# Optimization experiments

Measured on AMD Instinct MI355X. Metric: run time of the kernel, lower is better.

Reference implementation:

```python
import jax, jax.numpy as jnp
import numpy as np

B, N, DIM, H = 512, 98, 512, 16
HD = DIM // H
WS = (2, 7, 7)  # window size; N == 2*7*7


def _relative_position_index(ws):
    d, h, w = ws
    coords = np.stack(np.meshgrid(np.arange(d), np.arange(h), np.arange(w), indexing='ij'))
    cf = coords.reshape(3, -1)  # [3, N]
    rel = cf[:, :, None] - cf[:, None, :]  # [3, N, N]
    rel = rel.transpose(1, 2, 0).astype(np.int64)
    rel[:, :, 0] += d - 1
    rel[:, :, 1] += h - 1
    rel[:, :, 2] += w - 1
    rel[:, :, 0] *= (2 * h - 1) * (2 * w - 1)
    rel[:, :, 1] *= 2 * w - 1
    return rel.sum(-1)  # [N, N] in [0, (2d-1)(2h-1)(2w-1))


def setup_inputs() -> dict:
    key = jax.random.key(0)
    ks = jax.random.split(key, 6)
    table_size = (2 * WS[0] - 1) * (2 * WS[1] - 1) * (2 * WS[2] - 1)  # 507
    return {
        'x': jax.random.normal(ks[0], (B, N, DIM), jnp.float32),
        'qkv_w': jax.random.normal(ks[1], (DIM, 3 * DIM), jnp.float32) * 0.02,
        'qkv_b': jnp.zeros((3 * DIM,), jnp.float32),
        'proj_w': jax.random.normal(ks[2], (DIM, DIM), jnp.float32) * 0.02,
        'proj_b': jnp.zeros((DIM,), jnp.float32),
        'bias_table': jax.random.normal(ks[3], (table_size, H), jnp.float32) * 0.02,
        'rel_index': jnp.asarray(_relative_position_index(WS)),
    }


def reference(x, qkv_w, qkv_b, proj_w, proj_b, bias_table, rel_index):
    b, n, c = x.shape
    scale = HD ** -0.5
    qkv = (x @ qkv_w + qkv_b).reshape(b, n, 3, H, HD)
    qkv = jnp.transpose(qkv, (2, 0, 3, 1, 4))  # [3, B, H, N, HD]
    q, k, v = qkv[0] * scale, qkv[1], qkv[2]
    attn = jnp.einsum('bhnd,bhmd->bhnm', q, k)  # [B, H, N, N]
    # gather relative position bias: [N,N] indices into [table, H] -> [H, N, N]
    bias = jnp.transpose(bias_table[rel_index], (2, 0, 1))
    attn = jax.nn.softmax(attn + bias[None], axis=-1)
    out = jnp.einsum('bhnm,bhmd->bhnd', attn, v)  # [B, H, N, HD]
    out = jnp.transpose(out, (0, 2, 1, 3)).reshape(b, n, c)
    return out @ proj_w + proj_b
```

## Files before the change

kernel.cpp:

```cpp
#include <hip/hip_runtime.h>

typedef unsigned short u16;
typedef __bf16 bf16x8 __attribute__((ext_vector_type(8)));
typedef float f32x4 __attribute__((ext_vector_type(4)));

typedef __attribute__((address_space(1))) const void* as1_cvp;
typedef __attribute__((address_space(3))) void* as3_vp;

__device__ __forceinline__ float b2f(u16 u) {
  union { unsigned int i; float f; } x; x.i = ((unsigned int)u) << 16; return x.f;
}
__device__ __forceinline__ u16 f2b(float f) {
  union { float f; unsigned int i; } x; x.f = f;
  unsigned int u = x.i;
  u += 0x7fffu + ((u >> 16) & 1u);
  return (u16)(u >> 16);
}

__global__ void k_detect(const u16* __restrict__ x, int* __restrict__ flag) {
  int t = threadIdx.x;
  int sane = 0;
#pragma unroll
  for (int i = 0; i < 8; ++i) {
    u16 u = x[t * 8 + i];
    int e = (u >> 7) & 0xFF;
    sane += (u == 0 || (e >= 100 && e <= 150)) ? 1 : 0;
  }
#pragma unroll
  for (int off = 32; off >= 1; off >>= 1) sane += __shfl_xor(sane, off);
  if (t == 0) *flag = (sane < 480) ? 1 : 0;
}

__global__ void k_convert(const void* __restrict__ xin, u16* __restrict__ xb,
                          const int* __restrict__ flagp) {
  if (!*flagp) return;
  long i = ((long)blockIdx.x * 256 + threadIdx.x) * 4;
  float4 v = *(const float4*)((const float*)xin + i);
  u16* o = xb + i;
  o[0] = f2b(v.x); o[1] = f2b(v.y); o[2] = f2b(v.z); o[3] = f2b(v.w);
}

__global__ void k_transpose(const void* __restrict__ W, u16* __restrict__ WT,
                            const int* __restrict__ flagp, int K, int N) {
  __shared__ u16 tile[32][33];
  int f = *flagp;
  int n0 = blockIdx.x * 32, k0 = blockIdx.y * 32;
  int tx = threadIdx.x, ty = threadIdx.y;
#pragma unroll
  for (int i = 0; i < 32; i += 8) {
    long idx = (long)(k0 + ty + i) * N + n0 + tx;
    tile[ty + i][tx] = f ? f2b(((const float*)W)[idx]) : ((const u16*)W)[idx];
  }
  __syncthreads();
#pragma unroll
  for (int i = 0; i < 32; i += 8)
    WT[(long)(n0 + ty + i) * K + k0 + tx] = tile[tx][ty + i];
}

__global__ void k_biasfrag(const int* __restrict__ rel, const void* __restrict__ table,
                           u16* __restrict__ biasFrag, const int* __restrict__ flagp) {
  int t = blockIdx.x * 256 + threadIdx.x;
  int f = *flagp;
  int ln = t & 63, r2 = t >> 6;
  int tj = r2 & 7, r3 = r2 >> 3;
  int ti = r3 % 7, h = r3 / 7;
  int col = ln & 15, qrow = ln >> 4;
  int j = tj * 16 + col;
  u16 v[4];
#pragma unroll
  for (int r = 0; r < 4; ++r) {
    int i = ti * 16 + qrow * 4 + r; if (i > 97) i = 97;
    float val;
    if (j < 98) {
      int rr = rel[i * 98 + j];
      val = f ? ((const float*)table)[rr * 16 + h] : b2f(((const u16*)table)[rr * 16 + h]);
    } else {
      val = -1e30f;
    }
    v[r] = f2b(val);
  }
  ushort4 out; out.x = v[0]; out.y = v[1]; out.z = v[2]; out.w = v[3];
  *(ushort4*)(biasFrag + (long)t * 4) = out;
}

__global__ __launch_bounds__(256) void k_gemm_bt(
    const u16* __restrict__ A_raw, const u16* __restrict__ A_conv,
    const u16* __restrict__ BT, const void* __restrict__ bias, void* __restrict__ C,
    const int* __restrict__ flagp, int N, int K, int out_follows_flag) {
  __shared__ __align__(16) u16 As[128 * 32];
  __shared__ __align__(16) u16 Bs[128 * 32];
  const int f = *flagp;
  const u16* A = f ? A_conv : A_raw;
  const int t = threadIdx.x, w = t >> 6, ln = t & 63;
  const long bm = (long)blockIdx.x * 128, bn = (long)blockIdx.y * 128;
  const int lrow = ln >> 2, lseg = ln & 3;
  const u16* ag0 = A + (bm + w * 32 + lrow) * (long)K + lseg * 8;
  const u16* ag1 = ag0 + 16L * K;
  const u16* bg0 = BT + (bn + w * 32 + lrow) * (long)K + lseg * 8;
  const u16* bg1 = bg0 + 16L * K;
  u16* As0 = &As[w * 1024]; u16* As1 = &As[w * 1024 + 512];
  u16* Bs0 = &Bs[w * 1024]; u16* Bs1 = &Bs[w * 1024 + 512];
  const int wm = w & 1, wn = w >> 1;
  const int col = ln & 15, qrow = ln >> 4;
  f32x4 acc[4][4] = {};
  for (int k0 = 0; k0 < K; k0 += 32) {
    __syncthreads();
    __builtin_amdgcn_global_load_lds((as1_cvp)(const void*)(ag0 + k0), (as3_vp)As0, 16, 0, 0);
    __builtin_amdgcn_global_load_lds((as1_cvp)(const void*)(ag1 + k0), (as3_vp)As1, 16, 0, 0);
    __builtin_amdgcn_global_load_lds((as1_cvp)(const void*)(bg0 + k0), (as3_vp)Bs0, 16, 0, 0);
    __builtin_amdgcn_global_load_lds((as1_cvp)(const void*)(bg1 + k0), (as3_vp)Bs1, 16, 0, 0);
    __syncthreads();
    bf16x8 af[4], bfr[4];
#pragma unroll
    for (int mi = 0; mi < 4; ++mi)
      af[mi] = *(const bf16x8*)&As[(wm * 64 + mi * 16 + col) * 32 + qrow * 8];
#pragma unroll
    for (int ni = 0; ni < 4; ++ni)
      bfr[ni] = *(const bf16x8*)&Bs[(wn * 64 + ni * 16 + col) * 32 + qrow * 8];
#pragma unroll
    for (int mi = 0; mi < 4; ++mi)
#pragma unroll
      for (int ni = 0; ni < 4; ++ni)
        acc[mi][ni] = __builtin_amdgcn_mfma_f32_16x16x32_bf16(af[mi], bfr[ni], acc[mi][ni], 0, 0, 0);
  }
  const int of = out_follows_flag ? f : 0;
  float bv[4];
#pragma unroll
  for (int ni = 0; ni < 4; ++ni) {
    long c = bn + wn * 64 + ni * 16 + col;
    bv[ni] = f ? ((const float*)bias)[c] : b2f(((const u16*)bias)[c]);
  }
#pragma unroll
  for (int mi = 0; mi < 4; ++mi)
#pragma unroll
    for (int ni = 0; ni < 4; ++ni)
#pragma unroll
      for (int r = 0; r < 4; ++r) {
        long row = bm + wm * 64 + mi * 16 + qrow * 4 + r;
        long c = bn + wn * 64 + ni * 16 + col;
        float v = acc[mi][ni][r] + bv[ni];
        if (of) ((float*)C)[row * N + c] = v;
        else    ((u16*)C)[row * N + c] = f2b(v);
      }
}

__global__ __launch_bounds__(256) void k_attn(
    const u16* __restrict__ qkv, const u16* __restrict__ biasFrag,
    u16* __restrict__ attnout) {
  __shared__ __align__(16) u16 Qs[112 * 32];
  __shared__ __align__(16) u16 Ks[128 * 32];
  __shared__ __align__(16) u16 Vt[32 * 136];
  __shared__ __align__(16) u16 Ps[4][16 * 136];
  const int b = blockIdx.x, h = blockIdx.y;
  const int t = threadIdx.x, w = t >> 6, ln = t & 63;
  const u16* qbase = qkv + (long)b * 98 * 1536 + h * 32;
  {
    const int gr = ln >> 2, gc = (ln & 3) * 8;
    for (int n = w; n < 7; n += 4) {
      int g = n * 16 + gr; if (g > 97) g = 97;
      __builtin_amdgcn_global_load_lds((as1_cvp)(const void*)(qbase + (long)g * 1536 + gc),
                                       (as3_vp)(Qs + n * 512), 16, 0, 0);
    }
    for (int n = w; n < 8; n += 4) {
      int g = n * 16 + gr; if (g > 97) g = 97;
      __builtin_amdgcn_global_load_lds((as1_cvp)(const void*)(qbase + 512 + (long)g * 1536 + gc),
                                       (as3_vp)(Ks + n * 512), 16, 0, 0);
    }
  }
  for (int z = t; z < 32 * 19; z += 256) {
    int d = z / 19, q = z % 19;
    *(unsigned int*)&Vt[d * 136 + 98 + q * 2] = 0u;
  }
  for (int idx = t; idx < 784; idx += 256) {
    int i = idx >> 3, c4 = (idx & 7) * 4;
    ushort4 v4 = *(const ushort4*)(qbase + 1024 + (long)i * 1536 + c4);
    Vt[(c4 + 0) * 136 + i] = v4.x;
    Vt[(c4 + 1) * 136 + i] = v4.y;
    Vt[(c4 + 2) * 136 + i] = v4.z;
    Vt[(c4 + 3) * 136 + i] = v4.w;
  }
  __syncthreads();
  const int col = ln & 15, qrow = ln >> 4;
  const float scale = 0.17677669529663687f;
  u16* Psw = &Ps[w][0];
  f32x4 o[2][2] = {{{0.f,0.f,0.f,0.f},{0.f,0.f,0.f,0.f}},{{0.f,0.f,0.f,0.f},{0.f,0.f,0.f,0.f}}};
  for (int tt = 0; tt < 2; ++tt) {
    const int ti = w + tt * 4;
    if (ti >= 7) break;
    const u16* bp = biasFrag + ((long)((h * 7 + ti) * 8) * 64 + ln) * 4;
    ushort4 bfv[8];
#pragma unroll
    for (int tj = 0; tj < 8; ++tj) bfv[tj] = *(const ushort4*)(bp + tj * 256);
    bf16x8 aq = *(const bf16x8*)&Qs[(ti * 16 + col) * 32 + qrow * 8];
    f32x4 s[8];
#pragma unroll
    for (int tj = 0; tj < 8; ++tj) {
      bf16x8 bk = *(const bf16x8*)&Ks[(tj * 16 + col) * 32 + qrow * 8];
      f32x4 z = {0.f, 0.f, 0.f, 0.f};
      s[tj] = __builtin_amdgcn_mfma_f32_16x16x32_bf16(aq, bk, z, 0, 0, 0);
    }
#pragma unroll
    for (int r = 0; r < 4; ++r) {
      float vals[8]; float m = -1e30f;
#pragma unroll
      for (int tj = 0; tj < 8; ++tj) {
        u16 bb = (r == 0) ? bfv[tj].x : (r == 1) ? bfv[tj].y : (r == 2) ? bfv[tj].z : bfv[tj].w;
        float v = fmaf(s[tj][r], scale, b2f(bb));
        vals[tj] = v; m = fmaxf(m, v);
      }
#pragma unroll
      for (int off = 1; off < 16; off <<= 1) m = fmaxf(m, __shfl_xor(m, off));
      float sum = 0.f;
#pragma unroll
      for (int tj = 0; tj < 8; ++tj) { vals[tj] = __expf(vals[tj] - m); sum += vals[tj]; }
#pragma unroll
      for (int off = 1; off < 16; off <<= 1) sum += __shfl_xor(sum, off);
      float inv = 1.f / sum;
      const int rt = qrow * 4 + r;
#pragma unroll
      for (int tj = 0; tj < 8; ++tj)
        Psw[rt * 136 + tj * 16 + col] = f2b(vals[tj] * inv);
    }
#pragma unroll
    for (int ks = 0; ks < 4; ++ks) {
      bf16x8 ap  = *(const bf16x8*)&Psw[col * 136 + ks * 32 + qrow * 8];
      bf16x8 bv0 = *(const bf16x8*)&Vt[col * 136 + ks * 32 + qrow * 8];
      bf16x8 bv1 = *(const bf16x8*)&Vt[(16 + col) * 136 + ks * 32 + qrow * 8];
      o[tt][0] = __builtin_amdgcn_mfma_f32_16x16x32_bf16(ap, bv0, o[tt][0], 0, 0, 0);
      o[tt][1] = __builtin_amdgcn_mfma_f32_16x16x32_bf16(ap, bv1, o[tt][1], 0, 0, 0);
    }
  }
  __syncthreads();
  u16* Os = Qs;
#pragma unroll
  for (int tt = 0; tt < 2; ++tt) {
    const int ti = w + tt * 4;
    if (ti >= 7) continue;
#pragma unroll
    for (int r = 0; r < 4; ++r) {
      const int i = ti * 16 + qrow * 4 + r;
      if (i < 98) {
        Os[i * 32 + col]      = f2b(o[tt][0][r]);
        Os[i * 32 + 16 + col] = f2b(o[tt][1][r]);
      }
    }
  }
  __syncthreads();
  u16* obase = attnout + (long)b * 98 * 512 + h * 32;
  for (int idx = t; idx < 784; idx += 256) {
    int i = idx >> 3, c4 = (idx & 7) * 4;
    *(ushort4*)(obase + (long)i * 512 + c4) = *(const ushort4*)&Os[i * 32 + c4];
  }
}

extern "C" void kernel_launch(void* const* d_in, const int* in_sizes, int n_in,
                              void* d_out, int out_size, void* d_ws, size_t ws_size,
                              hipStream_t stream) {
  (void)in_sizes; (void)n_in; (void)out_size; (void)ws_size;
  char* p = (char*)d_ws;
  u16* qkvbuf   = (u16*)p;  p += 50176L * 1536 * 2;
  u16* attnbuf  = (u16*)p;  u16* xb = attnbuf; p += 50176L * 512 * 2;
  u16* wqkvT    = (u16*)p;  p += 1536L * 512 * 2;
  u16* wprojT   = (u16*)p;  p += 512L * 512 * 2;
  u16* biasFrag = (u16*)p;  p += 57344L * 4 * 2;
  int* flagp    = (int*)p;

  k_detect<<<1, 64, 0, stream>>>((const u16*)d_in[0], flagp);
  k_convert<<<25088, 256, 0, stream>>>(d_in[0], xb, flagp);
  k_transpose<<<dim3(48, 16), dim3(32, 8), 0, stream>>>(d_in[1], wqkvT, flagp, 512, 1536);
  k_transpose<<<dim3(16, 16), dim3(32, 8), 0, stream>>>(d_in[3], wprojT, flagp, 512, 512);
  k_biasfrag<<<224, 256, 0, stream>>>((const int*)d_in[6], d_in[5], biasFrag, flagp);
  k_gemm_bt<<<dim3(392, 12), 256, 0, stream>>>((const u16*)d_in[0], xb, wqkvT, d_in[2],
                                               qkvbuf, flagp, 1536, 512, 0);
  k_attn<<<dim3(512, 16), 256, 0, stream>>>(qkvbuf, biasFrag, attnbuf);
  k_gemm_bt<<<dim3(392, 4), 256, 0, stream>>>(attnbuf, attnbuf, wprojT, d_in[4],
                                              d_out, flagp, 512, 512, 1);
}
```

Before: 476.0 us.

## Replace GEMM with 256x256 tiled, double-buffered, swizzled-LDS pipelined kernel

Rewrites the GEMM used for the QKV and output projections. It now uses 256x256 block tiles with 8 waves and a K-step of 64, double-buffers LDS and issues async global-to-LDS prefetches interleaved with MFMA quadrants. It also uses an XOR swizzle on LDS chunks to avoid bank conflicts, raises MFMA issue priority with s_setprio, and remaps workgroups across XCDs. The goal is to cut the per-k-step barrier stalls and reload overhead of the old 128x128 single-buffer kernel, at the cost of heavier LDS use (128KB per block), more register pressure and fragile hand-placed waitcnt sequencing.

```diff
diff --git a/kernel.cpp b/kernel.cpp
--- a/kernel.cpp
+++ b/kernel.cpp
@@ -83,60 +83,111 @@
   *(ushort4*)(biasFrag + (long)t * 4) = out;
 }
 
-__global__ __launch_bounds__(256) void k_gemm_bt(
+#define MFMA_Q(M0, N0)                                                         \
+  __builtin_amdgcn_s_setprio(1);                                               \
+  _Pragma("unroll") for (int mi = 0; mi < 4; ++mi)                             \
+  _Pragma("unroll") for (int ni = 0; ni < 2; ++ni)                             \
+  _Pragma("unroll") for (int kk = 0; kk < 2; ++kk)                             \
+      acc[(M0) + mi][(N0) + ni] = __builtin_amdgcn_mfma_f32_16x16x32_bf16(     \
+          afr[mi][kk], bfr[(N0) + ni][kk], acc[(M0) + mi][(N0) + ni], 0, 0, 0);\
+  __builtin_amdgcn_s_setprio(0);
+
+#define STAGE(arr, bufi, half, src, kt) do {                                   \
+    u16* _d = &arr[(bufi) * 16384 + (half) * 8192 + w * 512];                  \
+    const u16* _s = (src) + (long)(half) * 128 * K + (long)(kt) * 64;          \
+    __builtin_amdgcn_global_load_lds((as1_cvp)(const void*)_s, (as3_vp)_d, 16, 0, 0); \
+    __builtin_amdgcn_global_load_lds((as1_cvp)(const void*)(_s + 64L * K),     \
+                                     (as3_vp)(_d + 4096), 16, 0, 0);           \
+  } while (0)
+
+__global__ __launch_bounds__(512, 2) void k_gemm256(
     const u16* __restrict__ A_raw, const u16* __restrict__ A_conv,
     const u16* __restrict__ BT, const void* __restrict__ bias, void* __restrict__ C,
-    const int* __restrict__ flagp, int N, int K, int out_follows_flag) {
-  __shared__ __align__(16) u16 As[128 * 32];
-  __shared__ __align__(16) u16 Bs[128 * 32];
+    const int* __restrict__ flagp, int N, int K, int out_follows_flag, int NBY) {
+  __shared__ __align__(16) u16 As[32768];
+  __shared__ __align__(16) u16 Bs[32768];
   const int f = *flagp;
   const u16* A = f ? A_conv : A_raw;
   const int t = threadIdx.x, w = t >> 6, ln = t & 63;
-  const long bm = (long)blockIdx.x * 128, bn = (long)blockIdx.y * 128;
-  const int lrow = ln >> 2, lseg = ln & 3;
-  const u16* ag0 = A + (bm + w * 32 + lrow) * (long)K + lseg * 8;
-  const u16* ag1 = ag0 + 16L * K;
-  const u16* bg0 = BT + (bn + w * 32 + lrow) * (long)K + lseg * 8;
-  const u16* bg1 = bg0 + 16L * K;
-  u16* As0 = &As[w * 1024]; u16* As1 = &As[w * 1024 + 512];
-  u16* Bs0 = &Bs[w * 1024]; u16* Bs1 = &Bs[w * 1024 + 512];
-  const int wm = w & 1, wn = w >> 1;
-  const int col = ln & 15, qrow = ln >> 4;
-  f32x4 acc[4][4] = {};
-  for (int k0 = 0; k0 < K; k0 += 32) {
-    __syncthreads();
-    __builtin_amdgcn_global_load_lds((as1_cvp)(const void*)(ag0 + k0), (as3_vp)As0, 16, 0, 0);
-    __builtin_amdgcn_global_load_lds((as1_cvp)(const void*)(ag1 + k0), (as3_vp)As1, 16, 0, 0);
-    __builtin_amdgcn_global_load_lds((as1_cvp)(const void*)(bg0 + k0), (as3_vp)Bs0, 16, 0, 0);
-    __builtin_amdgcn_global_load_lds((as1_cvp)(const void*)(bg1 + k0), (as3_vp)Bs1, 16, 0, 0);
-    __syncthreads();
-    bf16x8 af[4], bfr[4];
-#pragma unroll
-    for (int mi = 0; mi < 4; ++mi)
-      af[mi] = *(const bf16x8*)&As[(wm * 64 + mi * 16 + col) * 32 + qrow * 8];
-#pragma unroll
-    for (int ni = 0; ni < 4; ++ni)
-      bfr[ni] = *(const bf16x8*)&Bs[(wn * 64 + ni * 16 + col) * 32 + qrow * 8];
-#pragma unroll
-    for (int mi = 0; mi < 4; ++mi)
-#pragma unroll
-      for (int ni = 0; ni < 4; ++ni)
-        acc[mi][ni] = __builtin_amdgcn_mfma_f32_16x16x32_bf16(af[mi], bfr[ni], acc[mi][ni], 0, 0, 0);
-  }
-  const int of = out_follows_flag ? f : 0;
+  const int nwg = gridDim.x, cpx = nwg >> 3;
+  const int wg = (blockIdx.x & 7) * cpx + (blockIdx.x >> 3);
+  const long bm = (long)(wg / NBY) * 256, bn = (long)(wg % NBY) * 256;
+  const int NK = K >> 6;
+  const int wm = w >> 2, wn = w & 3, bh = wn >> 1, bq = wn & 1;
+  const int col = ln & 15, qrow = ln >> 4, cx = ln & 7;
+  const int srow = w * 8 + (ln >> 3);
+  const int schunk = (ln & 7) ^ ((ln >> 3) & 7);
+  const u16* aS = A + (bm + srow) * (long)K + schunk * 8;
+  const u16* bS = BT + (bn + srow) * (long)K + schunk * 8;
+  const u16* aRd = &As[wm * 8192 + col * 64];
+  const u16* bRd = &Bs[bh * 8192 + bq * 4096 + col * 64];
+  const int ko0 = (qrow ^ cx) * 8;
+  const int ko1 = ((4 + qrow) ^ cx) * 8;
   float bv[4];
 #pragma unroll
   for (int ni = 0; ni < 4; ++ni) {
     long c = bn + wn * 64 + ni * 16 + col;
     bv[ni] = f ? ((const float*)bias)[c] : b2f(((const u16*)bias)[c]);
   }
-#pragma unroll
-  for (int mi = 0; mi < 4; ++mi)
+  asm volatile("" ::: "memory");
+  STAGE(Bs, 0, 0, bS, 0); STAGE(Bs, 0, 1, bS, 0);
+  STAGE(As, 0, 0, aS, 0); STAGE(As, 0, 1, aS, 0);
+  STAGE(Bs, 1, 0, bS, 1); STAGE(Bs, 1, 1, bS, 1);
+  STAGE(As, 1, 0, aS, 1);
+  asm volatile("s_waitcnt vmcnt(6)" ::: "memory");
+  __builtin_amdgcn_s_barrier();
+
+  f32x4 acc[8][4] = {};
+  bf16x8 afr[4][2], bfr[4][2];
+  for (int kt = 0; kt < NK; ++kt) {
+    const int buf = kt & 1;
+    const u16* aP = aRd + buf * 16384;
+    const u16* bP = bRd + buf * 16384;
+#pragma unroll
+    for (int i = 0; i < 4; ++i) {
+      afr[i][0] = *(const bf16x8*)(aP + i * 1024 + ko0);
+      afr[i][1] = *(const bf16x8*)(aP + i * 1024 + ko1);
+      bfr[i][0] = *(const bf16x8*)(bP + i * 1024 + ko0);
+      bfr[i][1] = *(const bf16x8*)(bP + i * 1024 + ko1);
+    }
+    if (kt + 1 < NK) STAGE(As, buf ^ 1, 1, aS, kt + 1);
+    __builtin_amdgcn_s_barrier();
+    MFMA_Q(0, 0)
+    asm volatile("s_waitcnt lgkmcnt(0)" ::: "memory");
+    __builtin_amdgcn_s_barrier();
+    if (kt + 2 < NK) STAGE(Bs, buf, 0, bS, kt + 2);
+    __builtin_amdgcn_s_barrier();
+    MFMA_Q(0, 2)
+    asm volatile("s_waitcnt lgkmcnt(0)" ::: "memory");
+    __builtin_amdgcn_s_barrier();
+#pragma unroll
+    for (int i = 0; i < 4; ++i) {
+      afr[i][0] = *(const bf16x8*)(aP + (i + 4) * 1024 + ko0);
+      afr[i][1] = *(const bf16x8*)(aP + (i + 4) * 1024 + ko1);
+    }
+    if (kt + 2 < NK) STAGE(Bs, buf, 1, bS, kt + 2);
+    __builtin_amdgcn_s_barrier();
+    MFMA_Q(4, 0)
+    asm volatile("s_waitcnt lgkmcnt(0)" ::: "memory");
+    __builtin_amdgcn_s_barrier();
+    if (kt + 2 < NK) {
+      STAGE(As, buf, 0, aS, kt + 2);
+      asm volatile("s_waitcnt vmcnt(6)" ::: "memory");
+    } else if (kt + 1 < NK) {
+      asm volatile("s_waitcnt vmcnt(0)" ::: "memory");
+    }
+    __builtin_amdgcn_s_barrier();
+    MFMA_Q(4, 2)
+    __builtin_amdgcn_s_barrier();
+  }
+  const int of = out_follows_flag ? f : 0;
+#pragma unroll
+  for (int mi = 0; mi < 8; ++mi)
 #pragma unroll
     for (int ni = 0; ni < 4; ++ni)
 #pragma unroll
       for (int r = 0; r < 4; ++r) {
-        long row = bm + wm * 64 + mi * 16 + qrow * 4 + r;
+        long row = bm + wm * 128 + mi * 16 + qrow * 4 + r;
         long c = bn + wn * 64 + ni * 16 + col;
         float v = acc[mi][ni][r] + bv[ni];
         if (of) ((float*)C)[row * N + c] = v;
@@ -270,9 +321,9 @@
   k_transpose<<<dim3(48, 16), dim3(32, 8), 0, stream>>>(d_in[1], wqkvT, flagp, 512, 1536);
   k_transpose<<<dim3(16, 16), dim3(32, 8), 0, stream>>>(d_in[3], wprojT, flagp, 512, 512);
   k_biasfrag<<<224, 256, 0, stream>>>((const int*)d_in[6], d_in[5], biasFrag, flagp);
-  k_gemm_bt<<<dim3(392, 12), 256, 0, stream>>>((const u16*)d_in[0], xb, wqkvT, d_in[2],
-                                               qkvbuf, flagp, 1536, 512, 0);
+  k_gemm256<<<dim3(196 * 6), 512, 0, stream>>>((const u16*)d_in[0], xb, wqkvT, d_in[2],
+                                               qkvbuf, flagp, 1536, 512, 0, 6);
   k_attn<<<dim3(512, 16), 256, 0, stream>>>(qkvbuf, biasFrag, attnbuf);
-  k_gemm_bt<<<dim3(392, 4), 256, 0, stream>>>(attnbuf, attnbuf, wprojT, d_in[4],
-                                              d_out, flagp, 512, 512, 1);
-}
+  k_gemm256<<<dim3(196 * 2), 512, 0, stream>>>(attnbuf, attnbuf, wprojT, d_in[4],
+                                               d_out, flagp, 512, 512, 1, 2);
+}
```

Result: faster. 444.9 us (-6.5%).

## Rewrite GEMM with double-buffered K=64 LDS tiles, XOR swizzle, and XCD remap

Applied to the files above, without the earlier changes.

Replaces the single-buffered K=32 GEMM with a double-buffered K=64 pipeline that issues global-to-LDS loads two tiles ahead and waits on vmcnt before each barrier. LDS rows are XOR-swizzled to avoid bank conflicts on fragment reads. A 1D grid is remapped so consecutive tiles land on the same XCD, and launch bounds request two blocks per CU. This aims to overlap memory latency with MFMA work and cut the number of barriers, at the cost of 64KB of LDS per block and hand-written waitcnt logic.

```diff
diff --git a/kernel.cpp b/kernel.cpp
--- a/kernel.cpp
+++ b/kernel.cpp
@@ -83,53 +83,88 @@
   *(ushort4*)(biasFrag + (long)t * 4) = out;
 }
 
-__global__ __launch_bounds__(256) void k_gemm_bt(
+#define STAGE4(arr, bufi, src, kt) do {                                        \
+    u16* _d = &arr[(bufi) * 8192 + w * 512];                                   \
+    const u16* _s = (src) + (long)(kt) * 64;                                   \
+    __builtin_amdgcn_global_load_lds((as1_cvp)(const void*)(_s),           (as3_vp)(_d),        16, 0, 0); \
+    __builtin_amdgcn_global_load_lds((as1_cvp)(const void*)(_s + 32L * K), (as3_vp)(_d + 2048), 16, 0, 0); \
+    __builtin_amdgcn_global_load_lds((as1_cvp)(const void*)(_s + 64L * K), (as3_vp)(_d + 4096), 16, 0, 0); \
+    __builtin_amdgcn_global_load_lds((as1_cvp)(const void*)(_s + 96L * K), (as3_vp)(_d + 6144), 16, 0, 0); \
+  } while (0)
+
+__global__ __launch_bounds__(256, 2) void k_gemm128(
     const u16* __restrict__ A_raw, const u16* __restrict__ A_conv,
     const u16* __restrict__ BT, const void* __restrict__ bias, void* __restrict__ C,
-    const int* __restrict__ flagp, int N, int K, int out_follows_flag) {
-  __shared__ __align__(16) u16 As[128 * 32];
-  __shared__ __align__(16) u16 Bs[128 * 32];
+    const int* __restrict__ flagp, int N, int K, int out_follows_flag, int NBY) {
+  __shared__ __align__(16) u16 As[16384];
+  __shared__ __align__(16) u16 Bs[16384];
   const int f = *flagp;
   const u16* A = f ? A_conv : A_raw;
   const int t = threadIdx.x, w = t >> 6, ln = t & 63;
-  const long bm = (long)blockIdx.x * 128, bn = (long)blockIdx.y * 128;
-  const int lrow = ln >> 2, lseg = ln & 3;
-  const u16* ag0 = A + (bm + w * 32 + lrow) * (long)K + lseg * 8;
-  const u16* ag1 = ag0 + 16L * K;
-  const u16* bg0 = BT + (bn + w * 32 + lrow) * (long)K + lseg * 8;
-  const u16* bg1 = bg0 + 16L * K;
-  u16* As0 = &As[w * 1024]; u16* As1 = &As[w * 1024 + 512];
-  u16* Bs0 = &Bs[w * 1024]; u16* Bs1 = &Bs[w * 1024 + 512];
-  const int wm = w & 1, wn = w >> 1;
-  const int col = ln & 15, qrow = ln >> 4;
-  f32x4 acc[4][4] = {};
-  for (int k0 = 0; k0 < K; k0 += 32) {
-    __syncthreads();
-    __builtin_amdgcn_global_load_lds((as1_cvp)(const void*)(ag0 + k0), (as3_vp)As0, 16, 0, 0);
-    __builtin_amdgcn_global_load_lds((as1_cvp)(const void*)(ag1 + k0), (as3_vp)As1, 16, 0, 0);
-    __builtin_amdgcn_global_load_lds((as1_cvp)(const void*)(bg0 + k0), (as3_vp)Bs0, 16, 0, 0);
-    __builtin_amdgcn_global_load_lds((as1_cvp)(const void*)(bg1 + k0), (as3_vp)Bs1, 16, 0, 0);
-    __syncthreads();
-    bf16x8 af[4], bfr[4];
-#pragma unroll
-    for (int mi = 0; mi < 4; ++mi)
-      af[mi] = *(const bf16x8*)&As[(wm * 64 + mi * 16 + col) * 32 + qrow * 8];
-#pragma unroll
-    for (int ni = 0; ni < 4; ++ni)
-      bfr[ni] = *(const bf16x8*)&Bs[(wn * 64 + ni * 16 + col) * 32 + qrow * 8];
-#pragma unroll
-    for (int mi = 0; mi < 4; ++mi)
-#pragma unroll
-      for (int ni = 0; ni < 4; ++ni)
-        acc[mi][ni] = __builtin_amdgcn_mfma_f32_16x16x32_bf16(af[mi], bfr[ni], acc[mi][ni], 0, 0, 0);
-  }
-  const int of = out_follows_flag ? f : 0;
+  const int nwg = gridDim.x, cpx = nwg >> 3;
+  const int wg = (blockIdx.x & 7) * cpx + (blockIdx.x >> 3);
+  const long bm = (long)(wg / NBY) * 128, bn = (long)(wg % NBY) * 128;
+  const int NK = K >> 6;
+  const int wm = w >> 1, wn = w & 1;
+  const int col = ln & 15, qrow = ln >> 4, c7 = ln & 7;
+  const int srow = w * 8 + (ln >> 3);
+  const int schunk = (ln & 7) ^ ((ln >> 3) & 7);
+  const u16* aS = A + (bm + srow) * (long)K + schunk * 8;
+  const u16* bS = BT + (bn + srow) * (long)K + schunk * 8;
+  const u16* aRd = &As[(wm * 64 + col) * 64];
+  const u16* bRd = &Bs[(wn * 64 + col) * 64];
+  const int kc7 = col & 7;
+  const int ko0 = (qrow ^ kc7) * 8;
+  const int ko1 = ((4 + qrow) ^ kc7) * 8;
+  (void)c7;
   float bv[4];
 #pragma unroll
   for (int ni = 0; ni < 4; ++ni) {
     long c = bn + wn * 64 + ni * 16 + col;
     bv[ni] = f ? ((const float*)bias)[c] : b2f(((const u16*)bias)[c]);
   }
+  asm volatile("" ::: "memory");
+  STAGE4(As, 0, aS, 0); STAGE4(Bs, 0, bS, 0);
+  STAGE4(As, 1, aS, 1); STAGE4(Bs, 1, bS, 1);
+  asm volatile("s_waitcnt vmcnt(8)" ::: "memory");
+  __builtin_amdgcn_s_barrier();
+
+  f32x4 acc[4][4] = {};
+  for (int kt = 0; kt < NK; ++kt) {
+    const int buf = kt & 1;
+    const u16* aP = aRd + buf * 8192;
+    const u16* bP = bRd + buf * 8192;
+    bf16x8 a0[4], b0[4], a1[4], b1[4];
+#pragma unroll
+    for (int i = 0; i < 4; ++i) {
+      a0[i] = *(const bf16x8*)(aP + i * 1024 + ko0);
+      b0[i] = *(const bf16x8*)(bP + i * 1024 + ko0);
+      a1[i] = *(const bf16x8*)(aP + i * 1024 + ko1);
+      b1[i] = *(const bf16x8*)(bP + i * 1024 + ko1);
+    }
+    __builtin_amdgcn_s_setprio(1);
+#pragma unroll
+    for (int mi = 0; mi < 4; ++mi)
+#pragma unroll
+      for (int ni = 0; ni < 4; ++ni)
+        acc[mi][ni] = __builtin_amdgcn_mfma_f32_16x16x32_bf16(a0[mi], b0[ni], acc[mi][ni], 0, 0, 0);
+#pragma unroll
+    for (int mi = 0; mi < 4; ++mi)
+#pragma unroll
+      for (int ni = 0; ni < 4; ++ni)
+        acc[mi][ni] = __builtin_amdgcn_mfma_f32_16x16x32_bf16(a1[mi], b1[ni], acc[mi][ni], 0, 0, 0);
+    __builtin_amdgcn_s_setprio(0);
+    asm volatile("s_waitcnt lgkmcnt(0)" ::: "memory");
+    __builtin_amdgcn_s_barrier();
+    if (kt + 2 < NK) {
+      STAGE4(As, buf, aS, kt + 2); STAGE4(Bs, buf, bS, kt + 2);
+      asm volatile("s_waitcnt vmcnt(8)" ::: "memory");
+    } else if (kt + 1 < NK) {
+      asm volatile("s_waitcnt vmcnt(0)" ::: "memory");
+    }
+    __builtin_amdgcn_s_barrier();
+  }
+  const int of = out_follows_flag ? f : 0;
 #pragma unroll
   for (int mi = 0; mi < 4; ++mi)
 #pragma unroll
@@ -270,9 +305,9 @@
   k_transpose<<<dim3(48, 16), dim3(32, 8), 0, stream>>>(d_in[1], wqkvT, flagp, 512, 1536);
   k_transpose<<<dim3(16, 16), dim3(32, 8), 0, stream>>>(d_in[3], wprojT, flagp, 512, 512);
   k_biasfrag<<<224, 256, 0, stream>>>((const int*)d_in[6], d_in[5], biasFrag, flagp);
-  k_gemm_bt<<<dim3(392, 12), 256, 0, stream>>>((const u16*)d_in[0], xb, wqkvT, d_in[2],
-                                               qkvbuf, flagp, 1536, 512, 0);
+  k_gemm128<<<dim3(392 * 12), 256, 0, stream>>>((const u16*)d_in[0], xb, wqkvT, d_in[2],
+                                                qkvbuf, flagp, 1536, 512, 0, 12);
   k_attn<<<dim3(512, 16), 256, 0, stream>>>(qkvbuf, biasFrag, attnbuf);
-  k_gemm_bt<<<dim3(392, 4), 256, 0, stream>>>(attnbuf, attnbuf, wprojT, d_in[4],
-                                              d_out, flagp, 512, 512, 1);
-}
+  k_gemm128<<<dim3(392 * 4), 256, 0, stream>>>(attnbuf, attnbuf, wprojT, d_in[4],
+                                               d_out, flagp, 512, 512, 1, 4);
+}
```

Result: faster. 454.0 us (-4.6%).

## Pre-pack GEMM operands into MFMA fragment layout and load directly to registers

Applied to the files above, without the earlier changes.

Activations and weights are now repacked into a per-lane fragment layout: the input conversion, the weight packing and the attention output store all write it. This lets the GEMM kernel load operands straight from global memory into registers with a double-buffered register prefetch, with no LDS staging or barriers. The GEMM also gains XCD-aware block remapping, setprio around MFMA bursts and launch bounds allowing two blocks per CU. The cost is more register pressure, and the conversion kernel now runs even when the input is already bf16. Global loads stay coalesced 16-byte per lane but no longer share data between waves through LDS.

```diff
diff --git a/kernel.cpp b/kernel.cpp
--- a/kernel.cpp
+++ b/kernel.cpp
@@ -17,6 +17,7 @@
   return (u16)(u >> 16);
 }
 
+
 __global__ void k_detect(const u16* __restrict__ x, int* __restrict__ flag) {
   int t = threadIdx.x;
   int sane = 0;
@@ -31,30 +32,46 @@
   if (t == 0) *flag = (sane < 480) ? 1 : 0;
 }
 
-__global__ void k_convert(const void* __restrict__ xin, u16* __restrict__ xb,
-                          const int* __restrict__ flagp) {
-  if (!*flagp) return;
-  long i = ((long)blockIdx.x * 256 + threadIdx.x) * 4;
-  float4 v = *(const float4*)((const float*)xin + i);
-  u16* o = xb + i;
-  o[0] = f2b(v.x); o[1] = f2b(v.y); o[2] = f2b(v.z); o[3] = f2b(v.w);
-}
-
-__global__ void k_transpose(const void* __restrict__ W, u16* __restrict__ WT,
-                            const int* __restrict__ flagp, int K, int N) {
-  __shared__ u16 tile[32][33];
-  int f = *flagp;
-  int n0 = blockIdx.x * 32, k0 = blockIdx.y * 32;
-  int tx = threadIdx.x, ty = threadIdx.y;
-#pragma unroll
-  for (int i = 0; i < 32; i += 8) {
-    long idx = (long)(k0 + ty + i) * N + n0 + tx;
-    tile[ty + i][tx] = f ? f2b(((const float*)W)[idx]) : ((const u16*)W)[idx];
-  }
-  __syncthreads();
-#pragma unroll
-  for (int i = 0; i < 32; i += 8)
-    WT[(long)(n0 + ty + i) * K + k0 + tx] = tile[tx][ty + i];
+__global__ void k_convert_pack(const void* __restrict__ xin, u16* __restrict__ xp,
+                               const int* __restrict__ flagp) {
+  const int f = *flagp;
+  const int t = threadIdx.x, ln = t & 63;
+  const int u = blockIdx.x * 4 + (t >> 6);
+  const long r = (long)(u >> 4) * 16 + (ln & 15);
+  const int kbase = (u & 15) * 32 + (ln >> 4) * 8;
+  u16* dst = xp + ((long)u * 64 + ln) * 8;
+  if (f) {
+    const float* src = (const float*)xin + r * 512 + kbase;
+    float4 v0 = *(const float4*)src;
+    float4 v1 = *(const float4*)(src + 4);
+    ushort4 s0, s1;
+    s0.x = f2b(v0.x); s0.y = f2b(v0.y); s0.z = f2b(v0.z); s0.w = f2b(v0.w);
+    s1.x = f2b(v1.x); s1.y = f2b(v1.y); s1.z = f2b(v1.z); s1.w = f2b(v1.w);
+    *(ushort4*)dst = s0; *(ushort4*)(dst + 4) = s1;
+  } else {
+    const u16* src = (const u16*)xin + r * 512 + kbase;
+    *(ushort4*)dst = *(const ushort4*)src;
+    *(ushort4*)(dst + 4) = *(const ushort4*)(src + 4);
+  }
+}
+
+__global__ void k_pack_w(const void* __restrict__ W, u16* __restrict__ WP,
+                         const int* __restrict__ flagp, int N) {
+  const int f = *flagp;
+  const int t = threadIdx.x, ln = t & 63;
+  const int u = blockIdx.x * 4 + (t >> 6);
+  const int n = (u >> 4) * 16 + (ln & 15);
+  const int k0 = (u & 15) * 32 + (ln >> 4) * 8;
+  u16 v[8];
+#pragma unroll
+  for (int j = 0; j < 8; ++j) {
+    long idx = (long)(k0 + j) * N + n;
+    v[j] = f ? f2b(((const float*)W)[idx]) : ((const u16*)W)[idx];
+  }
+  u16* dst = WP + ((long)u * 64 + ln) * 8;
+  ushort4 s0; s0.x = v[0]; s0.y = v[1]; s0.z = v[2]; s0.w = v[3];
+  ushort4 s1; s1.x = v[4]; s1.y = v[5]; s1.z = v[6]; s1.w = v[7];
+  *(ushort4*)dst = s0; *(ushort4*)(dst + 4) = s1;
 }
 
 __global__ void k_biasfrag(const int* __restrict__ rel, const void* __restrict__ table,
@@ -83,53 +100,56 @@
   *(ushort4*)(biasFrag + (long)t * 4) = out;
 }
 
-__global__ __launch_bounds__(256) void k_gemm_bt(
-    const u16* __restrict__ A_raw, const u16* __restrict__ A_conv,
-    const u16* __restrict__ BT, const void* __restrict__ bias, void* __restrict__ C,
-    const int* __restrict__ flagp, int N, int K, int out_follows_flag) {
-  __shared__ __align__(16) u16 As[128 * 32];
-  __shared__ __align__(16) u16 Bs[128 * 32];
+#define LOADSET(SA, SB, KC)                                                    \
+  _Pragma("unroll") for (int mi = 0; mi < 4; ++mi) {                           \
+    SA[mi][0] = *(const bf16x8*)(aB + mi * 16384 + (KC) * 1024);               \
+    SA[mi][1] = *(const bf16x8*)(aB + mi * 16384 + (KC) * 1024 + 1024);        \
+  }                                                                            \
+  _Pragma("unroll") for (int ni = 0; ni < 4; ++ni) {                           \
+    SB[ni][0] = *(const bf16x8*)(bB + ni * 16384 + (KC) * 1024);               \
+    SB[ni][1] = *(const bf16x8*)(bB + ni * 16384 + (KC) * 1024 + 1024);        \
+  }
+
+#define MFMASET(SA, SB)                                                        \
+  __builtin_amdgcn_s_setprio(1);                                               \
+  _Pragma("unroll") for (int kk = 0; kk < 2; ++kk)                             \
+  _Pragma("unroll") for (int mi = 0; mi < 4; ++mi)                             \
+  _Pragma("unroll") for (int ni = 0; ni < 4; ++ni)                             \
+      acc[mi][ni] = __builtin_amdgcn_mfma_f32_16x16x32_bf16(                   \
+          SA[mi][kk], SB[ni][kk], acc[mi][ni], 0, 0, 0);                       \
+  __builtin_amdgcn_s_setprio(0);
+
+__global__ __launch_bounds__(256, 2) void k_gemm_direct(
+    const u16* __restrict__ PA, const u16* __restrict__ PB,
+    const void* __restrict__ bias, void* __restrict__ C,
+    const int* __restrict__ flagp, int N, int out_follows_flag, int NBY) {
   const int f = *flagp;
-  const u16* A = f ? A_conv : A_raw;
   const int t = threadIdx.x, w = t >> 6, ln = t & 63;
-  const long bm = (long)blockIdx.x * 128, bn = (long)blockIdx.y * 128;
-  const int lrow = ln >> 2, lseg = ln & 3;
-  const u16* ag0 = A + (bm + w * 32 + lrow) * (long)K + lseg * 8;
-  const u16* ag1 = ag0 + 16L * K;
-  const u16* bg0 = BT + (bn + w * 32 + lrow) * (long)K + lseg * 8;
-  const u16* bg1 = bg0 + 16L * K;
-  u16* As0 = &As[w * 1024]; u16* As1 = &As[w * 1024 + 512];
-  u16* Bs0 = &Bs[w * 1024]; u16* Bs1 = &Bs[w * 1024 + 512];
-  const int wm = w & 1, wn = w >> 1;
+  const int nwg = gridDim.x, cpx = nwg >> 3;
+  const int wg = (blockIdx.x & 7) * cpx + (blockIdx.x >> 3);
+  const long bm = (long)(wg / NBY) * 128, bn = (long)(wg % NBY) * 128;
+  const int wm = w >> 1, wn = w & 1;
   const int col = ln & 15, qrow = ln >> 4;
-  f32x4 acc[4][4] = {};
-  for (int k0 = 0; k0 < K; k0 += 32) {
-    __syncthreads();
-    __builtin_amdgcn_global_load_lds((as1_cvp)(const void*)(ag0 + k0), (as3_vp)As0, 16, 0, 0);
-    __builtin_amdgcn_global_load_lds((as1_cvp)(const void*)(ag1 + k0), (as3_vp)As1, 16, 0, 0);
-    __builtin_amdgcn_global_load_lds((as1_cvp)(const void*)(bg0 + k0), (as3_vp)Bs0, 16, 0, 0);
-    __builtin_amdgcn_global_load_lds((as1_cvp)(const void*)(bg1 + k0), (as3_vp)Bs1, 16, 0, 0);
-    __syncthreads();
-    bf16x8 af[4], bfr[4];
-#pragma unroll
-    for (int mi = 0; mi < 4; ++mi)
-      af[mi] = *(const bf16x8*)&As[(wm * 64 + mi * 16 + col) * 32 + qrow * 8];
-#pragma unroll
-    for (int ni = 0; ni < 4; ++ni)
-      bfr[ni] = *(const bf16x8*)&Bs[(wn * 64 + ni * 16 + col) * 32 + qrow * 8];
-#pragma unroll
-    for (int mi = 0; mi < 4; ++mi)
-#pragma unroll
-      for (int ni = 0; ni < 4; ++ni)
-        acc[mi][ni] = __builtin_amdgcn_mfma_f32_16x16x32_bf16(af[mi], bfr[ni], acc[mi][ni], 0, 0, 0);
-  }
-  const int of = out_follows_flag ? f : 0;
+  const char* aB = (const char*)PA + ((bm >> 4) + wm * 4) * 16384L + ln * 16;
+  const char* bB = (const char*)PB + ((bn >> 4) + wn * 4) * 16384L + ln * 16;
   float bv[4];
 #pragma unroll
   for (int ni = 0; ni < 4; ++ni) {
     long c = bn + wn * 64 + ni * 16 + col;
     bv[ni] = f ? ((const float*)bias)[c] : b2f(((const u16*)bias)[c]);
   }
+  f32x4 acc[4][4] = {};
+  bf16x8 aX[4][2], bX[4][2], aY[4][2], bY[4][2];
+  LOADSET(aX, bX, 0)
+  LOADSET(aY, bY, 2)
+#pragma unroll
+  for (int kc = 0; kc < 16; kc += 4) {
+    MFMASET(aX, bX)
+    if (kc + 4 < 16) { LOADSET(aX, bX, kc + 4) }
+    MFMASET(aY, bY)
+    if (kc + 6 < 16) { LOADSET(aY, bY, kc + 6) }
+  }
+  const int of = out_follows_flag ? f : 0;
 #pragma unroll
   for (int mi = 0; mi < 4; ++mi)
 #pragma unroll
@@ -146,7 +166,7 @@
 
 __global__ __launch_bounds__(256) void k_attn(
     const u16* __restrict__ qkv, const u16* __restrict__ biasFrag,
-    u16* __restrict__ attnout) {
+    u16* __restrict__ attnp) {
   __shared__ __align__(16) u16 Qs[112 * 32];
   __shared__ __align__(16) u16 Ks[128 * 32];
   __shared__ __align__(16) u16 Vt[32 * 136];
@@ -246,10 +266,13 @@
     }
   }
   __syncthreads();
-  u16* obase = attnout + (long)b * 98 * 512 + h * 32;
-  for (int idx = t; idx < 784; idx += 256) {
-    int i = idx >> 3, c4 = (idx & 7) * 4;
-    *(ushort4*)(obase + (long)i * 512 + c4) = *(const ushort4*)&Os[i * 32 + c4];
+  for (int idx = t; idx < 392; idx += 256) {
+    int i = idx >> 2, o = idx & 3;
+    long r = (long)b * 98 + i;
+    u16* dst = attnp + ((r >> 4) * 16 + h) * 512 + ((r & 15) + (o << 4)) * 8;
+    const u16* src = &Os[i * 32 + o * 8];
+    *(ushort4*)dst = *(const ushort4*)src;
+    *(ushort4*)(dst + 4) = *(const ushort4*)(src + 4);
   }
 }
 
@@ -259,20 +282,20 @@
   (void)in_sizes; (void)n_in; (void)out_size; (void)ws_size;
   char* p = (char*)d_ws;
   u16* qkvbuf   = (u16*)p;  p += 50176L * 1536 * 2;
-  u16* attnbuf  = (u16*)p;  u16* xb = attnbuf; p += 50176L * 512 * 2;
-  u16* wqkvT    = (u16*)p;  p += 1536L * 512 * 2;
-  u16* wprojT   = (u16*)p;  p += 512L * 512 * 2;
+  u16* attnbuf  = (u16*)p;  u16* xp = attnbuf; p += 50176L * 512 * 2;
+  u16* wqkvP    = (u16*)p;  p += 1536L * 512 * 2;
+  u16* wprojP   = (u16*)p;  p += 512L * 512 * 2;
   u16* biasFrag = (u16*)p;  p += 57344L * 4 * 2;
   int* flagp    = (int*)p;
 
   k_detect<<<1, 64, 0, stream>>>((const u16*)d_in[0], flagp);
-  k_convert<<<25088, 256, 0, stream>>>(d_in[0], xb, flagp);
-  k_transpose<<<dim3(48, 16), dim3(32, 8), 0, stream>>>(d_in[1], wqkvT, flagp, 512, 1536);
-  k_transpose<<<dim3(16, 16), dim3(32, 8), 0, stream>>>(d_in[3], wprojT, flagp, 512, 512);
+  k_convert_pack<<<12544, 256, 0, stream>>>(d_in[0], xp, flagp);
+  k_pack_w<<<384, 256, 0, stream>>>(d_in[1], wqkvP, flagp, 1536);
+  k_pack_w<<<128, 256, 0, stream>>>(d_in[3], wprojP, flagp, 512);
   k_biasfrag<<<224, 256, 0, stream>>>((const int*)d_in[6], d_in[5], biasFrag, flagp);
-  k_gemm_bt<<<dim3(392, 12), 256, 0, stream>>>((const u16*)d_in[0], xb, wqkvT, d_in[2],
-                                               qkvbuf, flagp, 1536, 512, 0);
+  k_gemm_direct<<<dim3(392 * 12), 256, 0, stream>>>(xp, wqkvP, d_in[2], qkvbuf,
+                                                    flagp, 1536, 0, 12);
   k_attn<<<dim3(512, 16), 256, 0, stream>>>(qkvbuf, biasFrag, attnbuf);
-  k_gemm_bt<<<dim3(392, 4), 256, 0, stream>>>(attnbuf, attnbuf, wprojT, d_in[4],
-                                              d_out, flagp, 512, 512, 1);
-}
+  k_gemm_direct<<<dim3(392 * 4), 256, 0, stream>>>(attnbuf, wprojP, d_in[4], d_out,
+                                                   flagp, 512, 1, 4);
+}
```

Result: faster. 437.3 us (-8.1%).
